# Kernel tuning notes

Hardware: AMD Instinct MI355X
Metric: run time of the kernel (lower is better)

Reference implementation:

```python
import jax, jax.numpy as jnp
import numpy as np
from jax import lax

DN = ('NHWC', 'HWIO', 'NHWC')

def _conv(x, w):
    return lax.conv_general_dilated(x, w, window_strides=(1, 1), padding='SAME', dimension_numbers=DN)

def _hard_sigmoid(z):
    # keras hard_sigmoid: clip(0.2*z + 0.5, 0, 1) -- default recurrent_activation of ConvLSTM2D
    return jnp.clip(0.2 * z + 0.5, 0.0, 1.0)

def setup_inputs() -> dict:
    key = jax.random.key(0)
    ks = jax.random.split(key, 6)
    B, T, H, W, Cin = 4, 16, 64, 64, 32
    F, kh, kw = 64, 3, 3
    x  = jax.random.normal(ks[0], (B, T, H, W, Cin), dtype=jnp.float32)
    Wx = jax.random.normal(ks[1], (kh, kw, Cin, 4 * F), dtype=jnp.float32) * 0.05
    Wh = jax.random.normal(ks[2], (kh, kw, F, 4 * F), dtype=jnp.float32) * 0.05
    b  = jnp.zeros((4 * F,), dtype=jnp.float32)
    Wp = jax.random.normal(ks[3], (1, 1, Cin, F), dtype=jnp.float32) * 0.05
    bp = jnp.zeros((F,), dtype=jnp.float32)
    return {"x": x, "Wx": Wx, "Wh": Wh, "b": b, "Wp": Wp, "bp": bp}

def reference(x, Wx, Wh, b, Wp, bp):
    B, T, H, W, Cin = x.shape
    F = Wh.shape[2]
    # Precompute the input-to-gate convolutions for all timesteps at once.
    zx = _conv(x.reshape(B * T, H, W, Cin), Wx) + b          # (B*T, H, W, 4F)
    zx = zx.reshape(B, T, H, W, 4 * F).transpose(1, 0, 2, 3, 4)  # time-major

    def step(carry, zx_t):
        h, c = carry
        z = zx_t + _conv(h, Wh)                              # (B, H, W, 4F)
        zi, zf, zc, zo = jnp.split(z, 4, axis=-1)            # keras gate order i,f,c,o
        i = _hard_sigmoid(zi)
        f = _hard_sigmoid(zf)
        c_new = f * c + i * jnp.tanh(zc)
        o = _hard_sigmoid(zo)
        h_new = o * jnp.tanh(c_new)
        return (h_new, c_new), h_new

    h0 = jnp.zeros((B, H, W, F), dtype=x.dtype)
    c0 = jnp.zeros((B, H, W, F), dtype=x.dtype)
    _, hs = lax.scan(step, (h0, c0), zx)                     # (T, B, H, W, F)
    convlstm_out = hs.transpose(1, 0, 2, 3, 4)               # (B, T, H, W, F)

    # TimeDistributed 1x1 projection of the input as the residual branch.
    residual = _conv(x.reshape(B * T, H, W, Cin), Wp) + bp
    residual = residual.reshape(B, T, H, W, F)
    return convlstm_out + residual
```

## Files before the change

### kernel.cpp

```cpp
#include <hip/hip_runtime.h>

#define B_ 4
#define T_ 16
#define H_ 64
#define W_ 64
#define CIN 32
#define F_ 64
#define NCH 256
#define KSTEPS 27
#define NPHASE 14
#define WSTEP 10240
#define PHS   20480
#define TSLAB (H_ * W_ * F_)

#define OFF_H0 589824
#define OFF_H1 2686976

typedef __attribute__((ext_vector_type(8))) short short8;
typedef __attribute__((ext_vector_type(4))) float floatx4;
typedef __attribute__((address_space(3))) unsigned int  lds_u32;
typedef __attribute__((address_space(1))) const unsigned int g_u32;

__device__ __forceinline__ unsigned short f2bf(float f) {
  union { float f; unsigned u; } v; v.f = f;
  unsigned r = v.u + 0x7FFFu + ((v.u >> 16) & 1u);
  return (unsigned short)(r >> 16);
}

__device__ __forceinline__ float tanh_fast(float z) {
  float e = __expf(2.0f * z);
  return 1.0f - 2.0f * __builtin_amdgcn_rcpf(e + 1.0f);
}

__global__ void prep_weights(const float* __restrict__ Wx, const float* __restrict__ Wh,
                             unsigned short* __restrict__ WT) {
  int idx = blockIdx.x * 256 + threadIdx.x;
  int s = idx / WSTEP;
  int r = idx - s * WSTEP;
  int n = r / 40;
  int c = r - n * 40;
  unsigned short v = 0;
  if (c < 32 && s < KSTEPS) {
    int k  = s * 32 + c;
    int g  = k / 96;
    int ch = k - g * 96;
    float f = (ch < CIN) ? Wx[(g * CIN + ch) * NCH + n]
                         : Wh[(g * F_ + (ch - CIN)) * NCH + n];
    v = f2bf(f);
  }
  WT[idx] = v;
}

__global__ void prep_zero_h(float4* __restrict__ p) {
  int idx = blockIdx.x * 256 + threadIdx.x;
  p[idx] = make_float4(0.f, 0.f, 0.f, 0.f);
}

__global__ void prep_zero_c(float* __restrict__ out) {
  int idx = blockIdx.x * 256 + threadIdx.x;
  int b = idx >> 16;
  int i = idx & 65535;
  ((float4*)(out + (size_t)b * (T_ * TSLAB)))[i] = make_float4(0.f, 0.f, 0.f, 0.f);
}

__device__ __forceinline__ void stage_wt2(const unsigned short* __restrict__ src,
                                          short* dstbuf, int w, int lane) {
  __attribute__((address_space(3))) unsigned short* d =
      (__attribute__((address_space(3))) unsigned short*)dstbuf;
  const unsigned short* s = src + lane * 8;
  __builtin_amdgcn_global_load_lds((g_u32*)(s + w * 512),
                                   (lds_u32*)(d + w * 512), 16, 0, 0);
  __builtin_amdgcn_global_load_lds((g_u32*)(s + (w + 16) * 512),
                                   (lds_u32*)(d + (w + 16) * 512), 16, 0, 0);
  if (w < 8)
    __builtin_amdgcn_global_load_lds((g_u32*)(s + (w + 32) * 512),
                                     (lds_u32*)(d + (w + 32) * 512), 16, 0, 0);
}

__global__ __launch_bounds__(1024, 1)
void step_kernel(const float* __restrict__ x, const float* __restrict__ bias,
                 const float* __restrict__ Wp, const float* __restrict__ bp,
                 const unsigned short* __restrict__ WT,
                 const unsigned short* __restrict__ hprev,
                 unsigned short* __restrict__ hnew,
                 float* __restrict__ out, int t)
{
  __shared__ __align__(16) char smem[110208];
  short* patch = (short*)smem;
  short* bl0   = (short*)(smem + 28288);
  short* bl1   = (short*)(smem + 69248);
  float* gact  = (float*)smem;
  float* WpL   = (float*)(smem + 69632);

  const int tid  = threadIdx.x;
  const int w    = tid >> 6;
  const int lane = tid & 63;
  const int quad = lane >> 4;
  const int lr   = lane & 15;
  const int gate = w >> 2;
  const int mq   = w & 3;

  const int raw = blockIdx.x;
  const int bid = (raw & 7) * 32 + (raw >> 3);
  const int b   = bid >> 6;
  const int rem = bid & 63;
  const int y0  = (rem >> 1) << 1;
  const int x0  = (rem & 1) << 5;

  const int rot = bid % NPHASE;

  stage_wt2(WT + rot * PHS, bl0, w, lane);

  if (tid < 272) {
    int e = tid >> 1, half = tid & 1;
    int sy = e / 34, sx = e - sy * 34;
    int yy = y0 + sy - 1, xx = x0 + sx - 1;
    short* dst = patch + e * 104;
    bool in = (yy >= 0 && yy < H_ && xx >= 0 && xx < W_);
    if (half == 0) {
      if (in) {
        const float4* xs = (const float4*)(x + ((((b * T_ + t) * H_ + yy) * W_ + xx) * CIN));
        #pragma unroll
        for (int j = 0; j < 4; j++) {
          float4 f0 = xs[2 * j];
          float4 f1 = xs[2 * j + 1];
          union { short8 v; unsigned short u[8]; } pk;
          pk.u[0] = f2bf(f0.x); pk.u[1] = f2bf(f0.y); pk.u[2] = f2bf(f0.z); pk.u[3] = f2bf(f0.w);
          pk.u[4] = f2bf(f1.x); pk.u[5] = f2bf(f1.y); pk.u[6] = f2bf(f1.z); pk.u[7] = f2bf(f1.w);
          ((short8*)dst)[j] = pk.v;
        }
      } else {
        uint4 z = make_uint4(0, 0, 0, 0);
        uint4* d4 = (uint4*)dst;
        #pragma unroll
        for (int j = 0; j < 4; j++) d4[j] = z;
      }
    } else {
      uint4* d2 = (uint4*)(dst + 32);
      if (in) {
        const uint4* hs = (const uint4*)(hprev + ((b * H_ + yy) * W_ + xx) * F_);
        #pragma unroll
        for (int j = 0; j < 8; j++) d2[j] = hs[j];
      } else {
        uint4 z = make_uint4(0, 0, 0, 0);
        #pragma unroll
        for (int j = 0; j < 8; j++) d2[j] = z;
      }
    }
  }

  float bias_r[4];
  #pragma unroll
  for (int nf = 0; nf < 4; nf++) bias_r[nf] = bias[gate * 64 + nf * 16 + lr];

  floatx4 acc[4];
  #pragma unroll
  for (int nf = 0; nf < 4; nf++) acc[nf] = (floatx4){0.f, 0.f, 0.f, 0.f};

  const int px = mq * 16 + lr;
  const int ty = px >> 5, tx = px & 31;

  __syncthreads();

  for (int p = 0; p < NPHASE; p++) {
    short* cur = (p & 1) ? bl1 : bl0;
    if (p < NPHASE - 1) {
      int qn = p + 1 + rot; if (qn >= NPHASE) qn -= NPHASE;
      stage_wt2(WT + qn * PHS, (p & 1) ? bl0 : bl1, w, lane);
    }
    int q = p + rot; if (q >= NPHASE) q -= NPHASE;
    #pragma unroll
    for (int half = 0; half < 2; half++) {
      int s = 2 * q + half;
      if (s < KSTEPS) {
        int g  = s / 3;
        int c0 = (s - g * 3) * 32;
        int dy = g / 3, dx = g - dy * 3;
        short8 afr = *(const short8*)(patch + ((ty + dy) * 34 + tx + dx) * 104 + c0 + quad * 8);
        #pragma unroll
        for (int nf = 0; nf < 4; nf++) {
          short8 bfr = *(const short8*)(cur + half * WSTEP + (gate * 64 + nf * 16 + lr) * 40 + quad * 8);
          acc[nf] = __builtin_amdgcn_mfma_f32_16x16x32_bf16(afr, bfr, acc[nf], 0, 0, 0);
        }
      }
    }
    __syncthreads();
  }

  #pragma unroll
  for (int nf = 0; nf < 4; nf++)
    #pragma unroll
    for (int r = 0; r < 4; r++) {
      int mm = quad * 4 + r;
      float z = acc[nf][r] + bias_r[nf];
      float a;
      if (gate == 2) a = tanh_fast(z);
      else {
        a = __builtin_fmaf(z, 0.2f, 0.5f);
        a = fminf(fmaxf(a, 0.f), 1.f);
      }
      gact[(gate * 64 + mq * 16 + mm) * 68 + nf * 16 + lr] = a;
    }
  if (tid < 512)
    ((float4*)WpL)[tid] = ((const float4*)Wp)[tid];

  const int mloc = tid >> 4;
  const int cb   = (tid & 15) * 4;
  const int tyo  = mloc >> 5, txo = mloc & 31;
  const int gy   = y0 + tyo, gx = x0 + txo;
  const int hbase   = ((b * H_ + gy) * W_ + gx) * F_ + cb;
  const int outbase = (((b * T_ + t) * H_ + gy) * W_ + gx) * F_ + cb;

  float xv[32];
  {
    const float4* xs = (const float4*)(x + ((((b * T_ + t) * H_ + gy) * W_ + gx) * CIN));
    #pragma unroll
    for (int j = 0; j < 8; j++) {
      float4 f = xs[j];
      xv[4 * j] = f.x; xv[4 * j + 1] = f.y; xv[4 * j + 2] = f.z; xv[4 * j + 3] = f.w;
    }
  }
  float4 co4 = *(const float4*)(out + outbase);

  __syncthreads();

  float res[4];
  #pragma unroll
  for (int j = 0; j < 4; j++) res[j] = bp[cb + j];
  #pragma unroll
  for (int ci = 0; ci < 32; ci++) {
    float xf = xv[ci];
    float4 wv = *(const float4*)(WpL + ci * 64 + cb);
    res[0] += xf * wv.x; res[1] += xf * wv.y; res[2] += xf * wv.z; res[3] += xf * wv.w;
  }

  float4 gi = *(const float4*)(gact + (0 * 64 + mloc) * 68 + cb);
  float4 gf = *(const float4*)(gact + (1 * 64 + mloc) * 68 + cb);
  float4 gg = *(const float4*)(gact + (2 * 64 + mloc) * 68 + cb);
  float4 go = *(const float4*)(gact + (3 * 64 + mloc) * 68 + cb);
  float cold[4] = {co4.x, co4.y, co4.z, co4.w};
  float iv[4] = {gi.x, gi.y, gi.z, gi.w};
  float fv[4] = {gf.x, gf.y, gf.z, gf.w};
  float gv[4] = {gg.x, gg.y, gg.z, gg.w};
  float ov[4] = {go.x, go.y, go.z, go.w};
  float cn4[4], h4[4];
  union { unsigned short hv[4]; uint2 q; } hu;
  #pragma unroll
  for (int e = 0; e < 4; e++) {
    float cn = fv[e] * cold[e] + iv[e] * gv[e];
    float h  = ov[e] * tanh_fast(cn);
    cn4[e] = cn; h4[e] = h;
    hu.hv[e] = f2bf(h);
  }
  if (t < T_ - 1)
    *(float4*)(out + outbase + TSLAB) = make_float4(cn4[0], cn4[1], cn4[2], cn4[3]);
  *(float4*)(out + outbase) = make_float4(h4[0] + res[0], h4[1] + res[1],
                                          h4[2] + res[2], h4[3] + res[3]);
  *(uint2*)(hnew + hbase) = hu.q;
}

extern "C" void kernel_launch(void* const* d_in, const int* in_sizes, int n_in,
                              void* d_out, int out_size, void* d_ws, size_t ws_size,
                              hipStream_t stream) {
  const float* x    = (const float*)d_in[0];
  const float* Wx   = (const float*)d_in[1];
  const float* Wh   = (const float*)d_in[2];
  const float* bias = (const float*)d_in[3];
  const float* Wp   = (const float*)d_in[4];
  const float* bp   = (const float*)d_in[5];
  float* out = (float*)d_out;

  unsigned short* WT = (unsigned short*)d_ws;
  unsigned short* h0 = (unsigned short*)((char*)d_ws + OFF_H0);
  unsigned short* h1 = (unsigned short*)((char*)d_ws + OFF_H1);

  hipLaunchKernelGGL(prep_weights, dim3(1120), dim3(256), 0, stream, Wx, Wh, WT);
  hipLaunchKernelGGL(prep_zero_h, dim3(1024), dim3(256), 0, stream,
                     (float4*)((char*)d_ws + OFF_H0));
  hipLaunchKernelGGL(prep_zero_c, dim3(1024), dim3(256), 0, stream, out);

  for (int t = 0; t < T_; t++) {
    const unsigned short* hp = (t & 1) ? h1 : h0;
    unsigned short*       hn = (t & 1) ? h0 : h1;
    hipLaunchKernelGGL(step_kernel, dim3(256), dim3(1024), 0, stream,
                       x, bias, Wp, bp, WT, hp, hn, out, t);
  }
}
```

Baseline: 682.4 us.

## Stage weights via register loads into padded LDS instead of direct global-to-LDS

```diff
diff --git a/kernel.cpp b/kernel.cpp
--- a/kernel.cpp
+++ b/kernel.cpp
@@ -9,8 +9,10 @@
 #define NCH 256
 #define KSTEPS 27
 #define NPHASE 14
-#define WSTEP 10240
-#define PHS   20480
+#define WSTEP2 8192
+#define PHS2   16384
+#define LROW   36
+#define LHALF  9216
 #define TSLAB (H_ * W_ * F_)
 
 #define OFF_H0 589824
@@ -18,8 +20,6 @@
 
 typedef __attribute__((ext_vector_type(8))) short short8;
 typedef __attribute__((ext_vector_type(4))) float floatx4;
-typedef __attribute__((address_space(3))) unsigned int  lds_u32;
-typedef __attribute__((address_space(1))) const unsigned int g_u32;
 
 __device__ __forceinline__ unsigned short f2bf(float f) {
   union { float f; unsigned u; } v; v.f = f;
@@ -33,14 +33,14 @@
 }
 
 __global__ void prep_weights(const float* __restrict__ Wx, const float* __restrict__ Wh,
-                             unsigned short* __restrict__ WT) {
+                             unsigned short* __restrict__ WT2) {
   int idx = blockIdx.x * 256 + threadIdx.x;
-  int s = idx / WSTEP;
-  int r = idx - s * WSTEP;
-  int n = r / 40;
-  int c = r - n * 40;
+  int s = idx >> 13;
+  int r = idx & 8191;
+  int n = r >> 5;
+  int c = r & 31;
   unsigned short v = 0;
-  if (c < 32 && s < KSTEPS) {
+  if (s < KSTEPS) {
     int k  = s * 32 + c;
     int g  = k / 96;
     int ch = k - g * 96;
@@ -48,7 +48,7 @@
                          : Wh[(g * F_ + (ch - CIN)) * NCH + n];
     v = f2bf(f);
   }
-  WT[idx] = v;
+  WT2[idx] = v;
 }
 
 __global__ void prep_zero_h(float4* __restrict__ p) {
@@ -63,32 +63,18 @@
   ((float4*)(out + (size_t)b * (T_ * TSLAB)))[i] = make_float4(0.f, 0.f, 0.f, 0.f);
 }
 
-__device__ __forceinline__ void stage_wt2(const unsigned short* __restrict__ src,
-                                          short* dstbuf, int w, int lane) {
-  __attribute__((address_space(3))) unsigned short* d =
-      (__attribute__((address_space(3))) unsigned short*)dstbuf;
-  const unsigned short* s = src + lane * 8;
-  __builtin_amdgcn_global_load_lds((g_u32*)(s + w * 512),
-                                   (lds_u32*)(d + w * 512), 16, 0, 0);
-  __builtin_amdgcn_global_load_lds((g_u32*)(s + (w + 16) * 512),
-                                   (lds_u32*)(d + (w + 16) * 512), 16, 0, 0);
-  if (w < 8)
-    __builtin_amdgcn_global_load_lds((g_u32*)(s + (w + 32) * 512),
-                                     (lds_u32*)(d + (w + 32) * 512), 16, 0, 0);
-}
-
-__global__ __launch_bounds__(1024, 1)
+__global__ __launch_bounds__(1024, 4)
 void step_kernel(const float* __restrict__ x, const float* __restrict__ bias,
                  const float* __restrict__ Wp, const float* __restrict__ bp,
-                 const unsigned short* __restrict__ WT,
+                 const unsigned short* __restrict__ WT2,
                  const unsigned short* __restrict__ hprev,
                  unsigned short* __restrict__ hnew,
                  float* __restrict__ out, int t)
 {
-  __shared__ __align__(16) char smem[110208];
+  __shared__ __align__(16) char smem[102016];
   short* patch = (short*)smem;
-  short* bl0   = (short*)(smem + 28288);
-  short* bl1   = (short*)(smem + 69248);
+  short* wb0   = (short*)(smem + 28288);
+  short* wb1   = (short*)(smem + 65152);
   float* gact  = (float*)smem;
   float* WpL   = (float*)(smem + 69632);
 
@@ -109,7 +95,16 @@
 
   const int rot = bid % NPHASE;
 
-  stage_wt2(WT + rot * PHS, bl0, w, lane);
+  const int su    = 2 * tid;
+  const int shalf = su >> 10;
+  const int srow  = (su & 1023) >> 2;
+  const int squad = su & 3;
+  const int stW   = shalf * LHALF + srow * LROW + squad * 8;
+
+  const uint4* g0 = (const uint4*)(WT2 + rot * PHS2);
+  uint4 r0 = g0[su];
+  uint4 r1 = g0[su + 1];
+  __builtin_amdgcn_sched_barrier(0);
 
   if (tid < 272) {
     int e = tid >> 1, half = tid & 1;
@@ -160,13 +155,20 @@
   const int px = mq * 16 + lr;
   const int ty = px >> 5, tx = px & 31;
 
+  asm volatile("s_waitcnt vmcnt(0)" ::: "memory");
+  __builtin_amdgcn_sched_barrier(0);
+  { short* d = wb0 + stW; *(uint4*)d = r0; *(uint4*)(d + 8) = r1; }
   __syncthreads();
 
   for (int p = 0; p < NPHASE; p++) {
-    short* cur = (p & 1) ? bl1 : bl0;
+    short* cur = (p & 1) ? wb1 : wb0;
+    short* nxt = (p & 1) ? wb0 : wb1;
     if (p < NPHASE - 1) {
       int qn = p + 1 + rot; if (qn >= NPHASE) qn -= NPHASE;
-      stage_wt2(WT + qn * PHS, (p & 1) ? bl0 : bl1, w, lane);
+      const uint4* gs = (const uint4*)(WT2 + qn * PHS2);
+      r0 = gs[su];
+      r1 = gs[su + 1];
+      __builtin_amdgcn_sched_barrier(0);
     }
     int q = p + rot; if (q >= NPHASE) q -= NPHASE;
     #pragma unroll
@@ -179,10 +181,18 @@
         short8 afr = *(const short8*)(patch + ((ty + dy) * 34 + tx + dx) * 104 + c0 + quad * 8);
         #pragma unroll
         for (int nf = 0; nf < 4; nf++) {
-          short8 bfr = *(const short8*)(cur + half * WSTEP + (gate * 64 + nf * 16 + lr) * 40 + quad * 8);
+          short8 bfr = *(const short8*)(cur + half * LHALF + (gate * 64 + nf * 16 + lr) * LROW + quad * 8);
           acc[nf] = __builtin_amdgcn_mfma_f32_16x16x32_bf16(afr, bfr, acc[nf], 0, 0, 0);
         }
       }
+    }
+    __builtin_amdgcn_sched_barrier(0);
+    if (p < NPHASE - 1) {
+      asm volatile("s_waitcnt vmcnt(0)" ::: "memory");
+      __builtin_amdgcn_sched_barrier(0);
+      short* d = nxt + stW;
+      *(uint4*)d = r0;
+      *(uint4*)(d + 8) = r1;
     }
     __syncthreads();
   }
@@ -270,11 +280,11 @@
   const float* bp   = (const float*)d_in[5];
   float* out = (float*)d_out;
 
-  unsigned short* WT = (unsigned short*)d_ws;
+  unsigned short* WT2 = (unsigned short*)d_ws;
   unsigned short* h0 = (unsigned short*)((char*)d_ws + OFF_H0);
   unsigned short* h1 = (unsigned short*)((char*)d_ws + OFF_H1);
 
-  hipLaunchKernelGGL(prep_weights, dim3(1120), dim3(256), 0, stream, Wx, Wh, WT);
+  hipLaunchKernelGGL(prep_weights, dim3(896), dim3(256), 0, stream, Wx, Wh, WT2);
   hipLaunchKernelGGL(prep_zero_h, dim3(1024), dim3(256), 0, stream,
                      (float4*)((char*)d_ws + OFF_H0));
   hipLaunchKernelGGL(prep_zero_c, dim3(1024), dim3(256), 0, stream, out);
@@ -283,6 +293,6 @@
     const unsigned short* hp = (t & 1) ? h1 : h0;
     unsigned short*       hn = (t & 1) ? h0 : h1;
     hipLaunchKernelGGL(step_kernel, dim3(256), dim3(1024), 0, stream,
-                       x, bias, Wp, bp, WT, hp, hn, out, t);
-  }
-}
+                       x, bias, Wp, bp, WT2, hp, hn, out, t);
+  }
+}
```

Measured after the change: 1.487 ms. 118% more time.

## Double per-block tile to 4x32 pixels, halving blocks and weight restaging

Applied to the files above, without the earlier changes.

```diff
diff --git a/kernel.cpp b/kernel.cpp
--- a/kernel.cpp
+++ b/kernel.cpp
@@ -15,6 +15,13 @@
 
 #define OFF_H0 589824
 #define OFF_H1 2686976
+
+#define PATCH_B 0
+#define WB0_B   42496
+#define WB1_B   83456
+#define GACT_B  0
+#define WPL_B   139264
+#define SMEM_B  147456
 
 typedef __attribute__((ext_vector_type(8))) short short8;
 typedef __attribute__((ext_vector_type(4))) float floatx4;
@@ -85,12 +92,12 @@
                  unsigned short* __restrict__ hnew,
                  float* __restrict__ out, int t)
 {
-  __shared__ __align__(16) char smem[110208];
-  short* patch = (short*)smem;
-  short* bl0   = (short*)(smem + 28288);
-  short* bl1   = (short*)(smem + 69248);
-  float* gact  = (float*)smem;
-  float* WpL   = (float*)(smem + 69632);
+  __shared__ __align__(16) char smem[SMEM_B];
+  short* patch = (short*)(smem + PATCH_B);
+  short* wb0   = (short*)(smem + WB0_B);
+  short* wb1   = (short*)(smem + WB1_B);
+  float* gact  = (float*)(smem + GACT_B);
+  float* WpL   = (float*)(smem + WPL_B);
 
   const int tid  = threadIdx.x;
   const int w    = tid >> 6;
@@ -101,17 +108,17 @@
   const int mq   = w & 3;
 
   const int raw = blockIdx.x;
-  const int bid = (raw & 7) * 32 + (raw >> 3);
-  const int b   = bid >> 6;
-  const int rem = bid & 63;
-  const int y0  = (rem >> 1) << 1;
+  const int bid = (raw & 7) * 16 + (raw >> 3);
+  const int b   = bid >> 5;
+  const int rem = bid & 31;
+  const int y0  = (rem >> 1) << 2;
   const int x0  = (rem & 1) << 5;
 
   const int rot = bid % NPHASE;
 
-  stage_wt2(WT + rot * PHS, bl0, w, lane);
-
-  if (tid < 272) {
+  stage_wt2(WT + rot * PHS, wb0, w, lane);
+
+  if (tid < 408) {
     int e = tid >> 1, half = tid & 1;
     int sy = e / 34, sx = e - sy * 34;
     int yy = y0 + sy - 1, xx = x0 + sx - 1;
@@ -149,24 +156,20 @@
     }
   }
 
-  float bias_r[4];
+  floatx4 acc[2][4];
   #pragma unroll
-  for (int nf = 0; nf < 4; nf++) bias_r[nf] = bias[gate * 64 + nf * 16 + lr];
-
-  floatx4 acc[4];
-  #pragma unroll
-  for (int nf = 0; nf < 4; nf++) acc[nf] = (floatx4){0.f, 0.f, 0.f, 0.f};
-
-  const int px = mq * 16 + lr;
-  const int ty = px >> 5, tx = px & 31;
+  for (int mf = 0; mf < 2; mf++)
+    #pragma unroll
+    for (int nf = 0; nf < 4; nf++)
+      acc[mf][nf] = (floatx4){0.f, 0.f, 0.f, 0.f};
 
   __syncthreads();
 
   for (int p = 0; p < NPHASE; p++) {
-    short* cur = (p & 1) ? bl1 : bl0;
+    short* cur = (p & 1) ? wb1 : wb0;
     if (p < NPHASE - 1) {
       int qn = p + 1 + rot; if (qn >= NPHASE) qn -= NPHASE;
-      stage_wt2(WT + qn * PHS, (p & 1) ? bl0 : bl1, w, lane);
+      stage_wt2(WT + qn * PHS, (p & 1) ? wb0 : wb1, w, lane);
     }
     int q = p + rot; if (q >= NPHASE) q -= NPHASE;
     #pragma unroll
@@ -176,36 +179,48 @@
         int g  = s / 3;
         int c0 = (s - g * 3) * 32;
         int dy = g / 3, dx = g - dy * 3;
-        short8 afr = *(const short8*)(patch + ((ty + dy) * 34 + tx + dx) * 104 + c0 + quad * 8);
-        #pragma unroll
-        for (int nf = 0; nf < 4; nf++) {
-          short8 bfr = *(const short8*)(cur + half * WSTEP + (gate * 64 + nf * 16 + lr) * 40 + quad * 8);
-          acc[nf] = __builtin_amdgcn_mfma_f32_16x16x32_bf16(afr, bfr, acc[nf], 0, 0, 0);
+        #pragma unroll
+        for (int mf = 0; mf < 2; mf++) {
+          int px = mq * 32 + mf * 16 + lr;
+          int ty = px >> 5, tx = px & 31;
+          short8 afr = *(const short8*)(patch + ((ty + dy) * 34 + tx + dx) * 104 + c0 + quad * 8);
+          #pragma unroll
+          for (int nf = 0; nf < 4; nf++) {
+            short8 bfr = *(const short8*)(cur + half * WSTEP + (gate * 64 + nf * 16 + lr) * 40 + quad * 8);
+            acc[mf][nf] = __builtin_amdgcn_mfma_f32_16x16x32_bf16(afr, bfr, acc[mf][nf], 0, 0, 0);
+          }
         }
       }
     }
     __syncthreads();
   }
 
-  #pragma unroll
-  for (int nf = 0; nf < 4; nf++)
-    #pragma unroll
-    for (int r = 0; r < 4; r++) {
-      int mm = quad * 4 + r;
-      float z = acc[nf][r] + bias_r[nf];
-      float a;
-      if (gate == 2) a = tanh_fast(z);
-      else {
-        a = __builtin_fmaf(z, 0.2f, 0.5f);
-        a = fminf(fmaxf(a, 0.f), 1.f);
-      }
-      gact[(gate * 64 + mq * 16 + mm) * 68 + nf * 16 + lr] = a;
-    }
+  {
+    float bias_r[4];
+    #pragma unroll
+    for (int nf = 0; nf < 4; nf++) bias_r[nf] = bias[gate * 64 + nf * 16 + lr];
+    #pragma unroll
+    for (int mf = 0; mf < 2; mf++)
+      #pragma unroll
+      for (int nf = 0; nf < 4; nf++)
+        #pragma unroll
+        for (int r = 0; r < 4; r++) {
+          int mm = quad * 4 + r;
+          float z = acc[mf][nf][r] + bias_r[nf];
+          float a;
+          if (gate == 2) a = tanh_fast(z);
+          else {
+            a = __builtin_fmaf(z, 0.2f, 0.5f);
+            a = fminf(fmaxf(a, 0.f), 1.f);
+          }
+          gact[(gate * 128 + mq * 32 + mf * 16 + mm) * 68 + nf * 16 + lr] = a;
+        }
+  }
   if (tid < 512)
     ((float4*)WpL)[tid] = ((const float4*)Wp)[tid];
 
-  const int mloc = tid >> 4;
-  const int cb   = (tid & 15) * 4;
+  const int mloc = tid >> 3;
+  const int cb   = (tid & 7) * 8;
   const int tyo  = mloc >> 5, txo = mloc & 31;
   const int gy   = y0 + tyo, gx = x0 + txo;
   const int hbase   = ((b * H_ + gy) * W_ + gx) * F_ + cb;
@@ -220,43 +235,51 @@
       xv[4 * j] = f.x; xv[4 * j + 1] = f.y; xv[4 * j + 2] = f.z; xv[4 * j + 3] = f.w;
     }
   }
-  float4 co4 = *(const float4*)(out + outbase);
+  float4 co4[2];
+  co4[0] = *(const float4*)(out + outbase);
+  co4[1] = *(const float4*)(out + outbase + 4);
 
   __syncthreads();
 
-  float res[4];
+  float res[8];
   #pragma unroll
-  for (int j = 0; j < 4; j++) res[j] = bp[cb + j];
+  for (int j = 0; j < 8; j++) res[j] = bp[cb + j];
   #pragma unroll
   for (int ci = 0; ci < 32; ci++) {
     float xf = xv[ci];
-    float4 wv = *(const float4*)(WpL + ci * 64 + cb);
-    res[0] += xf * wv.x; res[1] += xf * wv.y; res[2] += xf * wv.z; res[3] += xf * wv.w;
-  }
-
-  float4 gi = *(const float4*)(gact + (0 * 64 + mloc) * 68 + cb);
-  float4 gf = *(const float4*)(gact + (1 * 64 + mloc) * 68 + cb);
-  float4 gg = *(const float4*)(gact + (2 * 64 + mloc) * 68 + cb);
-  float4 go = *(const float4*)(gact + (3 * 64 + mloc) * 68 + cb);
-  float cold[4] = {co4.x, co4.y, co4.z, co4.w};
-  float iv[4] = {gi.x, gi.y, gi.z, gi.w};
-  float fv[4] = {gf.x, gf.y, gf.z, gf.w};
-  float gv[4] = {gg.x, gg.y, gg.z, gg.w};
-  float ov[4] = {go.x, go.y, go.z, go.w};
-  float cn4[4], h4[4];
-  union { unsigned short hv[4]; uint2 q; } hu;
+    float4 w0 = *(const float4*)(WpL + ci * 64 + cb);
+    float4 w1 = *(const float4*)(WpL + ci * 64 + cb + 4);
+    res[0] += xf * w0.x; res[1] += xf * w0.y; res[2] += xf * w0.z; res[3] += xf * w0.w;
+    res[4] += xf * w1.x; res[5] += xf * w1.y; res[6] += xf * w1.z; res[7] += xf * w1.w;
+  }
+
+  union { unsigned short hv[8]; uint4 q; } hu;
   #pragma unroll
-  for (int e = 0; e < 4; e++) {
-    float cn = fv[e] * cold[e] + iv[e] * gv[e];
-    float h  = ov[e] * tanh_fast(cn);
-    cn4[e] = cn; h4[e] = h;
-    hu.hv[e] = f2bf(h);
-  }
-  if (t < T_ - 1)
-    *(float4*)(out + outbase + TSLAB) = make_float4(cn4[0], cn4[1], cn4[2], cn4[3]);
-  *(float4*)(out + outbase) = make_float4(h4[0] + res[0], h4[1] + res[1],
-                                          h4[2] + res[2], h4[3] + res[3]);
-  *(uint2*)(hnew + hbase) = hu.q;
+  for (int j4 = 0; j4 < 2; j4++) {
+    int jj = j4 * 4;
+    float4 gi = *(const float4*)(gact + (0 * 128 + mloc) * 68 + cb + jj);
+    float4 gf = *(const float4*)(gact + (1 * 128 + mloc) * 68 + cb + jj);
+    float4 gg = *(const float4*)(gact + (2 * 128 + mloc) * 68 + cb + jj);
+    float4 go = *(const float4*)(gact + (3 * 128 + mloc) * 68 + cb + jj);
+    float cold[4] = {co4[j4].x, co4[j4].y, co4[j4].z, co4[j4].w};
+    float iv[4] = {gi.x, gi.y, gi.z, gi.w};
+    float fv[4] = {gf.x, gf.y, gf.z, gf.w};
+    float gv[4] = {gg.x, gg.y, gg.z, gg.w};
+    float ov[4] = {go.x, go.y, go.z, go.w};
+    float cn4[4], h4[4];
+    #pragma unroll
+    for (int e = 0; e < 4; e++) {
+      float cn = fv[e] * cold[e] + iv[e] * gv[e];
+      float h  = ov[e] * tanh_fast(cn);
+      cn4[e] = cn; h4[e] = h;
+      hu.hv[jj + e] = f2bf(h);
+    }
+    if (t < T_ - 1)
+      *(float4*)(out + outbase + TSLAB + jj) = make_float4(cn4[0], cn4[1], cn4[2], cn4[3]);
+    *(float4*)(out + outbase + jj) = make_float4(h4[0] + res[jj + 0], h4[1] + res[jj + 1],
+                                                 h4[2] + res[jj + 2], h4[3] + res[jj + 3]);
+  }
+  *(uint4*)(hnew + hbase) = hu.q;
 }
 
 extern "C" void kernel_launch(void* const* d_in, const int* in_sizes, int n_in,
@@ -282,7 +305,7 @@
   for (int t = 0; t < T_; t++) {
     const unsigned short* hp = (t & 1) ? h1 : h0;
     unsigned short*       hn = (t & 1) ? h0 : h1;
-    hipLaunchKernelGGL(step_kernel, dim3(256), dim3(1024), 0, stream,
+    hipLaunchKernelGGL(step_kernel, dim3(128), dim3(1024), 0, stream,
                        x, bias, Wp, bp, WT, hp, hn, out, t);
   }
 }
```

Result: slower. 1.359 ms (+99.1%).
